# Kernel tuning notes

Measured on AMD Instinct MI355X. Metric: run time of the kernel, lower is better.

The kernel has to match this reference:

```python
import jax, jax.numpy as jnp
import numpy as np

N, E, U, L = 10000, 320000, 256, 3


def setup_inputs() -> dict:
    key = jax.random.key(0)
    ks = jax.random.split(key, 16)
    s = 0.05
    p = {}
    p["pos"] = jax.random.normal(ks[0], (N, 2), jnp.float32)
    p["edge_attr_in"] = jax.random.uniform(ks[1], (E, 1), jnp.float32)
    p["edge_index"] = jax.random.randint(ks[2], (2, E), 0, N)
    p["Wp"] = jax.random.normal(ks[3], (2, U), jnp.float32) * s
    p["bp"] = jnp.zeros((U,), jnp.float32)
    p["Wa"] = jax.random.normal(ks[4], (1, U), jnp.float32) * s
    p["ba"] = jnp.zeros((U,), jnp.float32)
    p["W1"] = jax.random.normal(ks[5], (L, U, U), jnp.float32) * s
    p["b1"] = jnp.zeros((L, U), jnp.float32)
    p["W2"] = jax.random.normal(ks[6], (L, U, U), jnp.float32) * s
    p["b2"] = jnp.zeros((L, U), jnp.float32)
    p["We"] = jax.random.normal(ks[7], (L + 1, U, U), jnp.float32) * s
    p["be"] = jnp.zeros((L + 1, U), jnp.float32)
    p["Ws"] = jax.random.normal(ks[8], (L + 1, U, U), jnp.float32) * s
    p["Wt"] = jax.random.normal(ks[9], (L + 1, U, U), jnp.float32) * s
    p["Wm1"] = jax.random.normal(ks[10], (U + 1, U // 2), jnp.float32) * s
    p["bm1"] = jnp.zeros((U // 2,), jnp.float32)
    p["alpha"] = 0.25 * jnp.ones((1,), jnp.float32)  # PReLU default slope
    p["Wm2"] = jax.random.normal(ks[11], (U // 2, 1), jnp.float32) * s
    p["bm2"] = jnp.zeros((1,), jnp.float32)
    return p


def _forward(pos, edge_attr_in, edge_index, Wp, bp, Wa, ba, W1, b1, W2, b2,
             We, be, Ws, Wt, Wm1, bm1, alpha, Wm2, bm2):
    src, dst = edge_index[0], edge_index[1]
    x = pos @ Wp + bp                      # [N, U]
    e = edge_attr_in @ Wa + ba             # [E, U]

    def edge_update(x, e, l):
        # ResEdgeLinear: residual edge update from endpoint nodes + edge feats
        return e + jax.nn.relu(e @ We[l] + x[src] @ Ws[l] + x[dst] @ Wt[l] + be[l])

    for l in range(L):
        # ResNodeConv: gated gather-linear-scatter with residual
        gate = jax.nn.sigmoid(e)                                   # [E, U]
        msg = gate * (x[src] @ W2[l] + b2[l])                      # [E, U]
        agg = jax.ops.segment_sum(msg, dst, num_segments=N)        # [N, U]
        x_new = x + jax.nn.relu(x @ W1[l] + b1[l] + agg)
        e_new = edge_update(x, e, l)  # simultaneous update: both use old (x, e)
        x, e = x_new, e_new
    e = edge_update(x, e, L)

    h = jnp.concatenate([e, edge_attr_in[:, :1]], axis=-1) @ Wm1 + bm1
    h = jnp.where(h > 0, h, alpha * h)  # PReLU
    return h @ Wm2 + bm2                # [E, 1] logits


def reference(pos, edge_attr_in, edge_index, Wp, bp, Wa, ba, W1, b1, W2, b2,
              We, be, Ws, Wt, Wm1, bm1, alpha, Wm2, bm2):
    return _forward(pos, edge_attr_in, edge_index, Wp, bp, Wa, ba, W1, b1,
                    W2, b2, We, be, Ws, Wt, Wm1, bm1, alpha, Wm2, bm2)
```

## Files before the change

kernel.cpp:

```cpp
#include <hip/hip_runtime.h>
#include <hip/hip_bf16.h>
#include <stdint.h>

#define N_NODES 10000
#define N_EDGES 320000

using bf16x8 = __attribute__((ext_vector_type(8))) short;
using fp32x4 = __attribute__((ext_vector_type(4))) float;
using u16x8 = __attribute__((ext_vector_type(8))) unsigned short;
using i32x4 = __attribute__((ext_vector_type(4))) int;

__device__ __forceinline__ float bf2f(unsigned short u) {
  union { unsigned int i; float f; } v; v.i = ((unsigned int)u) << 16; return v.f;
}
__device__ __forceinline__ unsigned short f2bf(float f) {
  union { float f; unsigned int i; } v; v.f = f;
  unsigned int x = v.i;
  x += 0x7fffu + ((x >> 16) & 1u);
  return (unsigned short)(x >> 16);
}
__device__ __forceinline__ unsigned int f2bf_pk(float lo, float hi) {
  __hip_bfloat162 h = __float22bfloat162_rn(float2{lo, hi});
  union { __hip_bfloat162 h; unsigned int u; } cv; cv.h = h; return cv.u;
}

#define A_POS 0
#define A_EA 20000
#define A_WP 340000
#define A_BP 340512
#define A_WA 340768
#define A_BA 341024
#define A_W1 341280
#define A_B1 537888
#define A_W2 538656
#define A_B2 735264
#define A_WE 736032
#define A_BE 998176
#define A_WS 999200
#define A_WT 1261344
#define A_WM1 1523488
#define A_BM1 1556384
#define A_AL 1556512
#define A_WM2 1556544
#define A_BM2 1556672
#define ARENA_USED 1556673
#define ARENA_TOT 1556736

__constant__ int g_off[19] = {A_POS, A_EA, A_WP, A_BP, A_WA, A_BA, A_W1, A_B1,
                              A_W2, A_B2, A_WE, A_BE, A_WS, A_WT, A_WM1,
                              A_BM1, A_AL, A_WM2, A_BM2};

struct Ptrs { const void* p[19]; };

__global__ void k_detect(const unsigned short* wpraw, int* flag, int* deg) {
  int i = blockIdx.x * 256 + threadIdx.x;
  if (i < N_NODES) deg[i] = 0;
  if (blockIdx.x == 0) {
    __shared__ int cnt;
    int tid = threadIdx.x;
    if (tid == 0) cnt = 0;
    __syncthreads();
    float v0 = bf2f(wpraw[tid]);
    float v1 = bf2f(wpraw[256 + tid]);
    int big = (fabsf(v0) > 100.f ? 1 : 0) + (fabsf(v1) > 100.f ? 1 : 0);
    atomicAdd(&cnt, big);
    __syncthreads();
    if (tid == 0) *flag = (cnt > 10) ? 1 : 0;
  }
}

__global__ void k_cast(Ptrs ptrs, const int* __restrict__ flag,
                       unsigned short* __restrict__ arena) {
  int a = blockIdx.x * 256 + threadIdx.x;
  if (a >= ARENA_USED) return;
  int z = 0;
#pragma unroll
  for (int j = 1; j < 19; ++j) if (a >= g_off[j]) z = j;
  int i = a - g_off[z];
  float v;
  if (*flag) v = ((const float*)ptrs.p[z])[i];
  else       v = bf2f(((const unsigned short*)ptrs.p[z])[i]);
  arena[a] = f2bf(v);
}

__global__ void k_prep(const unsigned short* __restrict__ arena,
                       unsigned short* nodeBT, unsigned short* WeT,
                       unsigned short* Wm1T, unsigned short* biascat) {
  int z = blockIdx.z;
  int i = blockIdx.x * 256 + threadIdx.x;
  if (z == 19) {
    if (i < 3072) {
      int l = i >> 10, j = i & 1023;
      unsigned short v = 0;
      if (j < 256) v = arena[A_B1 + l * 256 + j];
      else if (j < 512) v = arena[A_B2 + l * 256 + (j - 256)];
      biascat[i] = v;
    } else if (i < 3584) {
      biascat[i] = 0;
    }
    return;
  }
  const unsigned short* src; unsigned short* dst; int srcN = 256;
  if (z < 3)       {                 src = arena + A_W1 + z * 65536; dst = nodeBT + z * 262144; }
  else if (z < 6)  { int l = z - 3;  src = arena + A_W2 + l * 65536; dst = nodeBT + l * 262144 + 65536; }
  else if (z < 10) { int l = z - 6;  src = arena + A_WS + l * 65536;
                     dst = (l < 3) ? nodeBT + l * 262144 + 131072 : nodeBT + 786432; }
  else if (z < 14) { int l = z - 10; src = arena + A_WT + l * 65536;
                     dst = (l < 3) ? nodeBT + l * 262144 + 196608 : nodeBT + 786432 + 65536; }
  else if (z < 18) { int l = z - 14; src = arena + A_WE + l * 65536; dst = WeT + l * 65536; }
  else             { src = arena + A_WM1; dst = Wm1T; srcN = 128; }
  if (i < srcN * 256) {
    int k = i & 255, n = i >> 8;
    dst[i] = src[k * srcN + n];
  }
}

__global__ void k_pack(const unsigned short* __restrict__ src,
                       unsigned short* __restrict__ dst, int MT, int nchunks) {
  int c = blockIdx.x * 256 + threadIdx.x;
  if (c >= nchunks) return;
  int perg = MT * 512;
  int g = c / perg, r = c % perg;
  int ks = r / (64 * MT);
  int rem = r % (64 * MT);
  int mt = rem >> 6, lane = rem & 63;
  int q = lane >> 4, ll = lane & 15;
  int oc = g * (MT * 16) + (ll >> 2) * (MT * 4) + (ll & 3) + mt * 4;
  i32x4 v = *(const i32x4*)((const char*)src + ((long)oc << 9) + (ks << 6) + (q << 4));
  ((i32x4*)dst)[c] = v;
}

__global__ void k_init_x(const unsigned short* __restrict__ arena,
                         float* __restrict__ xf, unsigned short* __restrict__ xbf,
                         float* __restrict__ agg) {
  int n = blockIdx.x, c = threadIdx.x;
  float p0 = bf2f(arena[A_POS + 2 * n]), p1 = bf2f(arena[A_POS + 2 * n + 1]);
  float v = fmaf(p0, bf2f(arena[A_WP + c]),
                 fmaf(p1, bf2f(arena[A_WP + 256 + c]), bf2f(arena[A_BP + c])));
  long idx = ((long)n << 8) + c;
  xf[idx] = v;
  xbf[idx] = f2bf(v);
  agg[idx] = 0.f;
}

__global__ void k_hist(const int* __restrict__ dstA, int* __restrict__ deg) {
  int i = blockIdx.x * 256 + threadIdx.x;
  if (i < N_EDGES) {
    int d = dstA[i];
    if ((unsigned)d < N_NODES) atomicAdd(&deg[d], 1);
  }
}

__global__ void k_scan(const int* __restrict__ deg, int* __restrict__ rowptr,
                       int* __restrict__ cursor) {
  __shared__ int part[256];
  int tid = threadIdx.x;
  int base = tid * 40;
  int s = 0;
  for (int i = 0; i < 40; ++i) {
    int idx = base + i;
    if (idx < N_NODES) s += deg[idx];
  }
  part[tid] = s;
  __syncthreads();
  if (tid == 0) {
    int run = 0;
    for (int i = 0; i < 256; ++i) { int t = part[i]; part[i] = run; run += t; }
    rowptr[N_NODES] = run;
  }
  __syncthreads();
  int run = part[tid];
  for (int i = 0; i < 40; ++i) {
    int idx = base + i;
    if (idx < N_NODES) { rowptr[idx] = run; cursor[idx] = run; run += deg[idx]; }
  }
}

__global__ void k_fill(const int* __restrict__ dstA, const int* __restrict__ srcA,
                       const unsigned short* __restrict__ arena,
                       int* __restrict__ cursor, int* __restrict__ eid,
                       int* __restrict__ csrc, int* __restrict__ cdst,
                       unsigned short* __restrict__ eaC) {
  int i = blockIdx.x * 256 + threadIdx.x;
  if (i < N_EDGES) {
    int d = dstA[i]; if ((unsigned)d >= N_NODES) d = 0;
    int p = atomicAdd(&cursor[d], 1);
    if ((unsigned)p < N_EDGES) {
      eid[p] = i;
      int s = srcA[i]; if ((unsigned)s >= N_NODES) s = 0;
      csrc[p] = s;
      cdst[p] = d;
      eaC[p] = arena[A_EA + i];
    }
  }
}

#define SM_PITCH 528
#define XS_PITCH 144
#define EDGE_BLOCKS (N_EDGES / 128)

template <bool NT, int ROWS, int BLK>
__device__ __forceinline__ void stage_tile(char* smc, const unsigned short* src,
                                           long rowBase) {
  int tid = threadIdx.x;
#pragma unroll
  for (int it = 0; it < ROWS * 32 / BLK; ++it) {
    int lin = it * BLK + tid;
    int row = lin >> 5, g = lin & 31;
    const i32x4* p = (const i32x4*)((const char*)src + ((rowBase + row) << 9) + (g << 4));
    i32x4 v = NT ? __builtin_nontemporal_load(p) : *p;
    *(i32x4*)(smc + row * SM_PITCH + (g << 4)) = v;
  }
}

template <int MT, int NTT>
__device__ __forceinline__ void gemm_swap(const char* smc, const unsigned short* WTp,
                                          int colBase, fp32x4 (&acc)[MT][NTT]) {
  const int lane = threadIdx.x & 63;
  const int q = lane >> 4, ll = lane & 15;
  const char* wbase = (const char*)WTp + ((long)colBase << 9) + (lane << 4);
  __builtin_amdgcn_s_setprio(1);
#pragma unroll
  for (int ks = 0; ks < 8; ++ks) {
    bf16x8 a[MT];
#pragma unroll
    for (int mt = 0; mt < MT; ++mt)
      a[mt] = *(const bf16x8*)(wbase + ((long)(ks * MT + mt) << 10));
    bf16x8 b[NTT];
#pragma unroll
    for (int nt = 0; nt < NTT; ++nt)
      b[nt] = *(const bf16x8*)(smc + (nt * 16 + ll) * SM_PITCH + (ks << 6) + (q << 4));
#pragma unroll
    for (int mt = 0; mt < MT; ++mt)
#pragma unroll
      for (int nt = 0; nt < NTT; ++nt)
        acc[mt][nt] = __builtin_amdgcn_mfma_f32_16x16x32_bf16(a[mt], b[nt], acc[mt][nt], 0, 0, 0);
  }
  __builtin_amdgcn_s_setprio(0);
}

template <int NTT>
__device__ __forceinline__ void edge_epilogue_cx(
    char* smc, char* xsw, const fp32x4 (&acc)[4][NTT], const int* s_src,
    const int* s_dst, const unsigned short* XW, int xw_pitch, int xs_off,
    int xt_off, const unsigned short* bePtr, int colBase, int lane) {
  const int q = lane >> 4, ll = lane & 15;
  const int cb = colBase + q * 16;
  u16x8 be0 = *(const u16x8*)(bePtr + cb);
  u16x8 be1 = *(const u16x8*)(bePtr + cb + 8);
  const int prow = lane >> 3;
  const int ppc = lane & 7;
  const int pcol = xs_off + colBase + ppc * 8;
  u16x8 pfA = *(const u16x8*)(XW + (long)s_src[prow] * xw_pitch + pcol);
  u16x8 pfB = *(const u16x8*)(XW + (long)s_src[8 + prow] * xw_pitch + pcol);
#pragma unroll
  for (int nt = 0; nt < NTT; ++nt) {
    *(u16x8*)(xsw + prow * XS_PITCH + ppc * 16) = pfA;
    *(u16x8*)(xsw + (8 + prow) * XS_PITCH + ppc * 16) = pfB;
    if (nt + 1 < NTT) {
      int elA = (nt + 1) * 16 + prow;
      pfA = *(const u16x8*)(XW + (long)s_src[elA] * xw_pitch + pcol);
      pfB = *(const u16x8*)(XW + (long)s_src[elA + 8] * xw_pitch + pcol);
    }
    int el = nt * 16 + ll;
    int dn = s_dst[el];
    const unsigned short* xtrow = XW + (long)dn * xw_pitch + xt_off + cb;
    u16x8 xt0 = *(const u16x8*)(xtrow);
    u16x8 xt1 = *(const u16x8*)(xtrow + 8);
    u16x8 xs0 = *(const u16x8*)(xsw + ll * XS_PITCH + q * 32);
    u16x8 xs1 = *(const u16x8*)(xsw + ll * XS_PITCH + q * 32 + 16);
    u16x8* slot = (u16x8*)(smc + el * SM_PITCH + cb * 2);
    u16x8 er0 = slot[0], er1 = slot[1];
    float f[16];
#pragma unroll
    for (int mt = 0; mt < 4; ++mt)
#pragma unroll
      for (int r = 0; r < 4; ++r) {
        int i = mt * 4 + r;
        float xsv = bf2f(i < 8 ? xs0[i] : xs1[i - 8]);
        float xtv = bf2f(i < 8 ? xt0[i] : xt1[i - 8]);
        float erv = bf2f(i < 8 ? er0[i] : er1[i - 8]);
        float bev = bf2f(i < 8 ? be0[i] : be1[i - 8]);
        float v = acc[mt][nt][r] + xsv + xtv + bev;
        v = fmaxf(v, 0.f);
        f[i] = erv + v;
      }
    union { u16x8 v; unsigned int w[4]; } O0, O1;
#pragma unroll
    for (int p = 0; p < 4; ++p) {
      O0.w[p] = f2bf_pk(f[2 * p], f[2 * p + 1]);
      O1.w[p] = f2bf_pk(f[8 + 2 * p], f[9 + 2 * p]);
    }
    slot[0] = O0.v;
    slot[1] = O1.v;
  }
}

template <int MODE>
__global__ __launch_bounds__(256, 2) void k_fat(
    unsigned short* __restrict__ e, const unsigned short* __restrict__ WT_edge,
    const unsigned short* __restrict__ XW_edge,
    const unsigned short* __restrict__ bePtr, const unsigned short* __restrict__ arena,
    const unsigned short* __restrict__ eaC,
    const int* __restrict__ csrc, const int* __restrict__ cdst,
    const unsigned short* __restrict__ xbf, const unsigned short* __restrict__ WT_node,
    const unsigned short* __restrict__ bias, unsigned short* __restrict__ XW_out) {
  __shared__ int4 sm4[128 * 33];
  __shared__ int4 xsb4[4 * 2304 / 16];
  __shared__ int s_src[128];
  __shared__ int s_dst[128];
  char* smc = (char*)sm4;
  const int tid = threadIdx.x;
  const int wave = tid >> 6, lane = tid & 63;
  const int q = lane >> 4, ll = lane & 15;

  if (blockIdx.x < EDGE_BLOCKS) {
    const long tileBase = (long)blockIdx.x * 128;
    const int colBase = wave * 64;
    if (MODE == 0) {
#pragma unroll
      for (int it = 0; it < 16; ++it) {
        int lin = it * 256 + tid;
        int row = lin >> 5, g = lin & 31;
        float eav = bf2f(eaC[tileBase + row]);
        int c0 = g * 8;
        float f[8];
#pragma unroll
        for (int j = 0; j < 8; ++j)
          f[j] = fmaf(eav, bf2f(arena[A_WA + c0 + j]), bf2f(arena[A_BA + c0 + j]));
        union { bf16x8 v; unsigned int w[4]; } O;
#pragma unroll
        for (int p = 0; p < 4; ++p) O.w[p] = f2bf_pk(f[2 * p], f[2 * p + 1]);
        *(bf16x8*)(smc + row * SM_PITCH + (g << 4)) = O.v;
      }
    } else {
      stage_tile<true, 128, 256>(smc, e, tileBase);
    }
    if (tid < 128) {
      long edge = tileBase + tid;
      int s = csrc[edge]; if ((unsigned)s >= N_NODES) s = 0;
      int d = cdst[edge]; if ((unsigned)d >= N_NODES) d = 0;
      s_src[tid] = s;
      s_dst[tid] = d;
    }
    __syncthreads();

    fp32x4 acc[4][8];
#pragma unroll
    for (int mt = 0; mt < 4; ++mt)
#pragma unroll
      for (int nt = 0; nt < 8; ++nt) acc[mt][nt] = 0.f;
    gemm_swap<4, 8>(smc, WT_edge, colBase, acc);
    __syncthreads();

    edge_epilogue_cx<8>(smc, (char*)xsb4 + wave * 2304, acc, s_src, s_dst,
                        XW_edge, 1024, 512, 768, bePtr, colBase, lane);
    __syncthreads();

#pragma unroll
    for (int it = 0; it < 16; ++it) {
      int lin = it * 256 + tid;
      int row = lin >> 5, g = lin & 31;
      i32x4 v = *(const i32x4*)(smc + row * SM_PITCH + (g << 4));
      __builtin_nontemporal_store(v, (i32x4*)((char*)e + ((tileBase + row) << 9) + (g << 4)));
    }
  } else {
    int b = blockIdx.x - EDGE_BLOCKS;
    int bx = b % 79, by = b / 79;
    const long tileBase = (long)bx * 128;
#pragma unroll
    for (int it = 0; it < 16; ++it) {
      int lin = it * 256 + tid;
      int row = lin >> 5, g = lin & 31;
      long rg = tileBase + row;
      if (rg > N_NODES - 1) rg = N_NODES - 1;
      i32x4 v = *(const i32x4*)((const char*)xbf + (rg << 9) + (g << 4));
      *(i32x4*)(smc + row * SM_PITCH + (g << 4)) = v;
    }
    __syncthreads();
    fp32x4 acc[2][8];
#pragma unroll
    for (int mt = 0; mt < 2; ++mt)
#pragma unroll
      for (int nt = 0; nt < 8; ++nt) acc[mt][nt] = 0.f;
    const int colBase = by * 128 + wave * 32;
    gemm_swap<2, 8>(smc, WT_node, colBase, acc);

    const int cb = colBase + q * 8;
    u16x8 bs8 = *(const u16x8*)(bias + cb);
#pragma unroll
    for (int nt = 0; nt < 8; ++nt) {
      long nn = tileBase + nt * 16 + ll;
      if (nn >= N_NODES) continue;
      float f[8];
#pragma unroll
      for (int mt = 0; mt < 2; ++mt)
#pragma unroll
        for (int r = 0; r < 4; ++r) {
          int i = mt * 4 + r;
          f[i] = acc[mt][nt][r] + bf2f(bs8[i]);
        }
      union { u16x8 v; unsigned int w[4]; } O;
#pragma unroll
      for (int p = 0; p < 4; ++p) O.w[p] = f2bf_pk(f[2 * p], f[2 * p + 1]);
      *(u16x8*)(XW_out + nn * 1024 + cb) = O.v;
    }
  }
}

__global__ __launch_bounds__(256, 2) void k_edge_last2(
    const unsigned short* __restrict__ e, const unsigned short* __restrict__ WeT2,
    const unsigned short* __restrict__ WeT3,
    const unsigned short* __restrict__ XW2, const unsigned short* __restrict__ XW3,
    const unsigned short* __restrict__ arena, const unsigned short* __restrict__ eaC,
    const int* __restrict__ csrc, const int* __restrict__ cdst,
    const unsigned short* __restrict__ Wm1T, const int* __restrict__ eid,
    const int* __restrict__ flag, void* __restrict__ out) {
  __shared__ int4 sm4[128 * 33];
  __shared__ int4 xsb4[4 * 2304 / 16];
  __shared__ int s_src[128];
  __shared__ int s_dst[128];
  char* smc = (char*)sm4;
  const long tileBase = (long)blockIdx.x * 128;
  const int tid = threadIdx.x;
  const int wave = tid >> 6, lane = tid & 63;
  const int q = lane >> 4, ll = lane & 15;
  const int colBase = wave * 64;
  char* xsw = (char*)xsb4 + wave * 2304;

  stage_tile<true, 128, 256>(smc, e, tileBase);
  if (tid < 128) {
    long edge = tileBase + tid;
    int s = csrc[edge]; if ((unsigned)s >= N_NODES) s = 0;
    int d = cdst[edge]; if ((unsigned)d >= N_NODES) d = 0;
    s_src[tid] = s;
    s_dst[tid] = d;
  }
  __syncthreads();

  fp32x4 acc[4][8];
#pragma unroll
  for (int mt = 0; mt < 4; ++mt)
#pragma unroll
    for (int nt = 0; nt < 8; ++nt) acc[mt][nt] = 0.f;
  gemm_swap<4, 8>(smc, WeT2, colBase, acc);
  __syncthreads();
  edge_epilogue_cx<8>(smc, xsw, acc, s_src, s_dst, XW2, 1024, 512, 768,
                      arena + A_BE + 2 * 256, colBase, lane);
  __syncthreads();

#pragma unroll
  for (int mt = 0; mt < 4; ++mt)
#pragma unroll
    for (int nt = 0; nt < 8; ++nt) acc[mt][nt] = 0.f;
  gemm_swap<4, 8>(smc, WeT3, colBase, acc);
  __syncthreads();
  edge_epilogue_cx<8>(smc, xsw, acc, s_src, s_dst, XW3, 512, 0, 256,
                      arena + A_BE + 3 * 256, colBase, lane);
  __syncthreads();

  fp32x4 acc2[2][8];
#pragma unroll
  for (int mt = 0; mt < 2; ++mt)
#pragma unroll
    for (int nt = 0; nt < 8; ++nt) acc2[mt][nt] = 0.f;
  const int colBase2 = wave * 32;
  gemm_swap<2, 8>(smc, Wm1T, colBase2, acc2);

  const int cb2 = colBase2 + q * 8;
  float alphaf = bf2f(arena[A_AL]);
  float bmc[8], wl[8], w2c[8];
#pragma unroll
  for (int i = 0; i < 8; ++i) {
    bmc[i] = bf2f(arena[A_BM1 + cb2 + i]);
    wl[i] = bf2f(arena[A_WM1 + 32768 + cb2 + i]);
    w2c[i] = bf2f(arena[A_WM2 + cb2 + i]);
  }
  __syncthreads();
  float* part = (float*)smc;
#pragma unroll
  for (int nt = 0; nt < 8; ++nt) {
    int el = nt * 16 + ll;
    float eav = bf2f(eaC[tileBase + el]);
    float ps = 0.f;
#pragma unroll
    for (int mt = 0; mt < 2; ++mt)
#pragma unroll
      for (int r = 0; r < 4; ++r) {
        int i = mt * 4 + r;
        float h = acc2[mt][nt][r] + bmc[i] + eav * wl[i];
        h = (h > 0.f) ? h : alphaf * h;
        ps += h * w2c[i];
      }
    ps += __shfl_xor(ps, 16, 64);
    ps += __shfl_xor(ps, 32, 64);
    if (q == 0) part[el * 4 + wave] = ps;
  }
  __syncthreads();
  if (tid < 128) {
    float t = part[tid * 4] + part[tid * 4 + 1] + part[tid * 4 + 2] + part[tid * 4 + 3]
            + bf2f(arena[A_BM2]);
    long row = tileBase + tid;
    int oe = eid[row]; if ((unsigned)oe >= N_EDGES) oe = 0;
    if (*flag) ((float*)out)[oe] = t;
    else       ((unsigned short*)out)[oe] = f2bf(t);
  }
}

__global__ __launch_bounds__(256, 2) void k_node_gemm(
    const unsigned short* __restrict__ xbf, const unsigned short* __restrict__ WT,
    const unsigned short* __restrict__ bias, unsigned short* __restrict__ out,
    int out_pitch) {
  __shared__ int4 sm4[128 * 33];
  char* smc = (char*)sm4;
  const long tileBase = (long)blockIdx.x * 128;
  {
    int tid = threadIdx.x;
#pragma unroll
    for (int it = 0; it < 16; ++it) {
      int lin = it * 256 + tid;
      int row = lin >> 5, g = lin & 31;
      long rg = tileBase + row;
      if (rg > N_NODES - 1) rg = N_NODES - 1;
      i32x4 v = *(const i32x4*)((const char*)xbf + (rg << 9) + (g << 4));
      *(i32x4*)(smc + row * SM_PITCH + (g << 4)) = v;
    }
  }
  __syncthreads();
  fp32x4 acc[2][8];
#pragma unroll
  for (int mt = 0; mt < 2; ++mt)
#pragma unroll
    for (int nt = 0; nt < 8; ++nt) acc[mt][nt] = 0.f;
  const int tid = threadIdx.x, wave = tid >> 6, lane = tid & 63;
  const int q = lane >> 4, ll = lane & 15;
  const int colBase = blockIdx.y * 128 + wave * 32;
  gemm_swap<2, 8>(smc, WT, colBase, acc);

  const int cb = colBase + q * 8;
  u16x8 bs8 = *(const u16x8*)(bias + cb);
#pragma unroll
  for (int nt = 0; nt < 8; ++nt) {
    long nn = tileBase + nt * 16 + ll;
    if (nn >= N_NODES) continue;
    float f[8];
#pragma unroll
    for (int mt = 0; mt < 2; ++mt)
#pragma unroll
      for (int r = 0; r < 4; ++r) {
        int i = mt * 4 + r;
        f[i] = acc[mt][nt][r] + bf2f(bs8[i]);
      }
    union { u16x8 v; unsigned int w[4]; } O;
#pragma unroll
    for (int p = 0; p < 4; ++p) O.w[p] = f2bf_pk(f[2 * p], f[2 * p + 1]);
    *(u16x8*)(out + nn * out_pitch + cb) = O.v;
  }
}

template <bool FIRST>
__global__ void k_agg(const int* __restrict__ csrc, const int* __restrict__ cdst,
                      const unsigned short* __restrict__ e,
                      const unsigned short* __restrict__ eaC,
                      const unsigned short* __restrict__ arena,
                      const unsigned short* __restrict__ XW, int xw_pitch, int x2_off,
                      float* __restrict__ agg) {
  __shared__ int s_src[64];
  __shared__ int s_dst[64];
  const long base = (long)blockIdx.x * 64;
  const int c = threadIdx.x;
  if (c < 64) {
    long r = base + c;
    int s = csrc[r]; if ((unsigned)s >= N_NODES) s = 0;
    int d = cdst[r]; if ((unsigned)d >= N_NODES) d = 0;
    s_src[c] = s;
    s_dst[c] = d;
  }
  __syncthreads();
  float wac = 0.f, bac = 0.f;
  if (FIRST) { wac = bf2f(arena[A_WA + c]); bac = bf2f(arena[A_BA + c]); }
  float a = 0.f;
  int run = s_dst[0];
  for (int b8 = 0; b8 < 64; b8 += 8) {
    float evv[8], x2v[8];
#pragma unroll
    for (int j = 0; j < 8; ++j) {
      int row = b8 + j;
      if (FIRST) evv[j] = fmaf(bf2f(eaC[base + row]), wac, bac);
      else evv[j] = bf2f(__builtin_nontemporal_load(e + ((base + row) << 8) + c));
      x2v[j] = bf2f(XW[(long)s_src[row] * xw_pitch + x2_off + c]);
    }
#pragma unroll
    for (int j = 0; j < 8; ++j) {
      int d = s_dst[b8 + j];
      if (d != run) {
        atomicAdd(&agg[((long)run << 8) + c], a);
        a = 0.f;
        run = d;
      }
      float gate = 1.f / (1.f + __expf(-evv[j]));
      a = fmaf(gate, x2v[j], a);
    }
  }
  atomicAdd(&agg[((long)run << 8) + c], a);
}

__global__ void k_node_update(float* __restrict__ xf, unsigned short* __restrict__ xbf,
                              const unsigned short* __restrict__ XW,
                              float* __restrict__ agg) {
  int n = blockIdx.x, c = threadIdx.x;
  long idx = ((long)n << 8) + c;
  float av = agg[idx];
  agg[idx] = 0.f;
  float t = bf2f(XW[((long)n << 10) + c]) + av;
  float nx = xf[idx] + fmaxf(t, 0.f);
  xf[idx] = nx;
  xbf[idx] = f2bf(nx);
}

extern "C" void kernel_launch(void* const* d_in, const int* in_sizes, int n_in,
                              void* d_out, int out_size, void* d_ws, size_t ws_size,
                              hipStream_t stream) {
  const int* eidx = (const int*)d_in[2];
  const int* srcA = eidx;
  const int* dstA = eidx + N_EDGES;
  (void)in_sizes; (void)n_in; (void)out_size;

  char* ws = (char*)d_ws;
  size_t off = 0;
  auto alloc = [&](size_t bytes) -> char* {
    char* p = ws + off;
    off = (off + bytes + 255) & ~(size_t)255;
    return p;
  };
  unsigned short* e_buf   = (unsigned short*)alloc((size_t)N_EDGES * 256 * 2);
  float*          xf      = (float*)alloc((size_t)N_NODES * 256 * 4);
  unsigned short* xbf     = (unsigned short*)alloc((size_t)N_NODES * 256 * 2);
  unsigned short* XWa     = (unsigned short*)alloc((size_t)N_NODES * 1024 * 2);
  unsigned short* XWb     = (unsigned short*)alloc((size_t)N_NODES * 1024 * 2);
  unsigned short* XW3     = (unsigned short*)alloc((size_t)N_NODES * 512 * 2);
  float*          agg     = (float*)alloc((size_t)N_NODES * 256 * 4);
  unsigned short* nodeBT  = (unsigned short*)alloc((size_t)917504 * 2);
  unsigned short* WeT     = (unsigned short*)alloc((size_t)4 * 65536 * 2);
  unsigned short* Wm1T    = (unsigned short*)alloc((size_t)32768 * 2);
  unsigned short* nodeBTp = (unsigned short*)alloc((size_t)917504 * 2);
  unsigned short* WeTp    = (unsigned short*)alloc((size_t)4 * 65536 * 2);
  unsigned short* Wm1Tp   = (unsigned short*)alloc((size_t)32768 * 2);
  unsigned short* biascat = (unsigned short*)alloc((size_t)3584 * 2);
  unsigned short* arena   = (unsigned short*)alloc((size_t)ARENA_TOT * 2);
  int* deg    = (int*)alloc((size_t)N_NODES * 4);
  int* rowptr = (int*)alloc((size_t)(N_NODES + 1) * 4);
  int* cursor = (int*)alloc((size_t)N_NODES * 4);
  int* eid    = (int*)alloc((size_t)N_EDGES * 4);
  int* csrc   = (int*)alloc((size_t)N_EDGES * 4);
  int* cdst   = (int*)alloc((size_t)N_EDGES * 4);
  unsigned short* eaC = (unsigned short*)alloc((size_t)N_EDGES * 2);
  int* flag   = (int*)alloc(4);
  if (ws_size < off) return;

  Ptrs ptrs;
  {
    int map[19] = {0, 1, 3, 4, 5, 6, 7, 8, 9, 10, 11, 12, 13, 14, 15, 16, 17, 18, 19};
    for (int j = 0; j < 19; ++j) ptrs.p[j] = d_in[map[j]];
  }

  dim3 blk(256);
  k_detect<<<dim3(40), blk, 0, stream>>>((const unsigned short*)d_in[3], flag, deg);
  k_cast<<<dim3((ARENA_USED + 255) / 256), blk, 0, stream>>>(ptrs, flag, arena);
  k_prep<<<dim3(256, 1, 20), blk, 0, stream>>>(arena, nodeBT, WeT, Wm1T, biascat);
  k_pack<<<dim3(448), blk, 0, stream>>>(nodeBT, nodeBTp, 2, 114688);
  k_pack<<<dim3(128), blk, 0, stream>>>(WeT, WeTp, 4, 32768);
  k_pack<<<dim3(16),  blk, 0, stream>>>(Wm1T, Wm1Tp, 2, 4096);
  k_init_x<<<dim3(N_NODES), blk, 0, stream>>>(arena, xf, xbf, agg);
  k_hist<<<dim3(N_EDGES / 256), blk, 0, stream>>>(dstA, deg);
  k_scan<<<dim3(1), blk, 0, stream>>>(deg, rowptr, cursor);
  k_fill<<<dim3(N_EDGES / 256), blk, 0, stream>>>(dstA, srcA, arena, cursor, eid, csrc,
                                                  cdst, eaC);

  k_node_gemm<<<dim3(79, 8), blk, 0, stream>>>(xbf, nodeBTp, biascat, XWa, 1024);
  k_agg<true><<<dim3(N_EDGES / 64), blk, 0, stream>>>(csrc, cdst, e_buf, eaC, arena,
                                                      XWa, 1024, 256, agg);
  k_node_update<<<dim3(N_NODES), blk, 0, stream>>>(xf, xbf, XWa, agg);
  k_fat<0><<<dim3(EDGE_BLOCKS + 632), blk, 0, stream>>>(
      e_buf, WeTp, XWa, arena + A_BE, arena, eaC, csrc, cdst,
      xbf, nodeBTp + 262144, biascat + 1024, XWb);
  k_agg<false><<<dim3(N_EDGES / 64), blk, 0, stream>>>(csrc, cdst, e_buf, eaC, arena,
                                                       XWb, 1024, 256, agg);
  k_node_update<<<dim3(N_NODES), blk, 0, stream>>>(xf, xbf, XWb, agg);
  k_fat<1><<<dim3(EDGE_BLOCKS + 632), blk, 0, stream>>>(
      e_buf, WeTp + 65536, XWb, arena + A_BE + 256, arena, eaC, csrc, cdst,
      xbf, nodeBTp + 2 * 262144, biascat + 2048, XWa);
  k_agg<false><<<dim3(N_EDGES / 64), blk, 0, stream>>>(csrc, cdst, e_buf, eaC, arena,
                                                       XWa, 1024, 256, agg);
  k_node_update<<<dim3(N_NODES), blk, 0, stream>>>(xf, xbf, XWa, agg);
  k_node_gemm<<<dim3(79, 4), blk, 0, stream>>>(xbf, nodeBTp + 786432, biascat + 3072, XW3, 512);
  k_edge_last2<<<dim3(EDGE_BLOCKS), blk, 0, stream>>>(
      e_buf, WeTp + 2 * 65536, WeTp + 3 * 65536, XWa, XW3, arena, eaC,
      csrc, cdst, Wm1Tp, eid, flag, d_out);
}
```

Baseline: 789.1 us.

## Fuse edge layers 0 and 1 with in-tile gated aggregation, splitting node GEMMs out

Layer-0 and layer-1 edge updates now run in one kernel, with the edge tile kept in shared memory between the two edge GEMMs instead of being written to and re-read from global memory. The layer-1 gated message aggregation is done in the same kernel, using the freshly computed layer-1 edge features and run-length merged atomicAdds over the dst-sorted edges, which removes one k_agg launch and its reread of e. The node GEMMs that used to share the fat kernels now run as separate k_node_gemm launches. The cost is more atomics and gathers inside the fused kernel, and the loss of overlap between node and edge GEMMs.

New measurement: 777.1 us. Within noise of the previous version (-1.5%).

```diff
diff --git a/kernel.cpp b/kernel.cpp
--- a/kernel.cpp
+++ b/kernel.cpp
@@ -296,115 +296,102 @@
   }
 }
 
-template <int MODE>
-__global__ __launch_bounds__(256, 2) void k_fat(
-    unsigned short* __restrict__ e, const unsigned short* __restrict__ WT_edge,
-    const unsigned short* __restrict__ XW_edge,
-    const unsigned short* __restrict__ bePtr, const unsigned short* __restrict__ arena,
-    const unsigned short* __restrict__ eaC,
+__global__ __launch_bounds__(256, 2) void k_edge01(
+    unsigned short* __restrict__ e, const unsigned short* __restrict__ WeT0,
+    const unsigned short* __restrict__ WeT1,
+    const unsigned short* __restrict__ XWa, const unsigned short* __restrict__ XWb,
+    const unsigned short* __restrict__ arena, const unsigned short* __restrict__ eaC,
     const int* __restrict__ csrc, const int* __restrict__ cdst,
-    const unsigned short* __restrict__ xbf, const unsigned short* __restrict__ WT_node,
-    const unsigned short* __restrict__ bias, unsigned short* __restrict__ XW_out) {
+    float* __restrict__ agg) {
   __shared__ int4 sm4[128 * 33];
   __shared__ int4 xsb4[4 * 2304 / 16];
   __shared__ int s_src[128];
   __shared__ int s_dst[128];
   char* smc = (char*)sm4;
+  const long tileBase = (long)blockIdx.x * 128;
   const int tid = threadIdx.x;
   const int wave = tid >> 6, lane = tid & 63;
-  const int q = lane >> 4, ll = lane & 15;
-
-  if (blockIdx.x < EDGE_BLOCKS) {
-    const long tileBase = (long)blockIdx.x * 128;
-    const int colBase = wave * 64;
-    if (MODE == 0) {
-#pragma unroll
-      for (int it = 0; it < 16; ++it) {
-        int lin = it * 256 + tid;
-        int row = lin >> 5, g = lin & 31;
-        float eav = bf2f(eaC[tileBase + row]);
-        int c0 = g * 8;
-        float f[8];
-#pragma unroll
-        for (int j = 0; j < 8; ++j)
-          f[j] = fmaf(eav, bf2f(arena[A_WA + c0 + j]), bf2f(arena[A_BA + c0 + j]));
-        union { bf16x8 v; unsigned int w[4]; } O;
-#pragma unroll
-        for (int p = 0; p < 4; ++p) O.w[p] = f2bf_pk(f[2 * p], f[2 * p + 1]);
-        *(bf16x8*)(smc + row * SM_PITCH + (g << 4)) = O.v;
+  const int colBase = wave * 64;
+  char* xsw = (char*)xsb4 + wave * 2304;
+
+#pragma unroll
+  for (int it = 0; it < 16; ++it) {
+    int lin = it * 256 + tid;
+    int row = lin >> 5, g = lin & 31;
+    float eav = bf2f(eaC[tileBase + row]);
+    int c0 = g * 8;
+    float f[8];
+#pragma unroll
+    for (int j = 0; j < 8; ++j)
+      f[j] = fmaf(eav, bf2f(arena[A_WA + c0 + j]), bf2f(arena[A_BA + c0 + j]));
+    union { bf16x8 v; unsigned int w[4]; } O;
+#pragma unroll
+    for (int p = 0; p < 4; ++p) O.w[p] = f2bf_pk(f[2 * p], f[2 * p + 1]);
+    *(bf16x8*)(smc + row * SM_PITCH + (g << 4)) = O.v;
+  }
+  if (tid < 128) {
+    long edge = tileBase + tid;
+    int s = csrc[edge]; if ((unsigned)s >= N_NODES) s = 0;
+    int d = cdst[edge]; if ((unsigned)d >= N_NODES) d = 0;
+    s_src[tid] = s;
+    s_dst[tid] = d;
+  }
+  __syncthreads();
+
+  fp32x4 acc[4][8];
+#pragma unroll
+  for (int mt = 0; mt < 4; ++mt)
+#pragma unroll
+    for (int nt = 0; nt < 8; ++nt) acc[mt][nt] = 0.f;
+  gemm_swap<4, 8>(smc, WeT0, colBase, acc);
+  __syncthreads();
+  edge_epilogue_cx<8>(smc, xsw, acc, s_src, s_dst, XWa, 1024, 512, 768,
+                      arena + A_BE, colBase, lane);
+  __syncthreads();
+
+  {
+    const int c = tid;
+    float a = 0.f;
+    int run = s_dst[0];
+    for (int b8 = 0; b8 < 128; b8 += 8) {
+      float evv[8], x2v[8];
+#pragma unroll
+      for (int j = 0; j < 8; ++j) {
+        int row = b8 + j;
+        evv[j] = bf2f(*(const unsigned short*)(smc + row * SM_PITCH + c * 2));
+        x2v[j] = bf2f(XWb[(long)s_src[row] * 1024 + 256 + c]);
       }
-    } else {
-      stage_tile<true, 128, 256>(smc, e, tileBase);
-    }
-    if (tid < 128) {
-      long edge = tileBase + tid;
-      int s = csrc[edge]; if ((unsigned)s >= N_NODES) s = 0;
-      int d = cdst[edge]; if ((unsigned)d >= N_NODES) d = 0;
-      s_src[tid] = s;
-      s_dst[tid] = d;
-    }
-    __syncthreads();
-
-    fp32x4 acc[4][8];
-#pragma unroll
-    for (int mt = 0; mt < 4; ++mt)
-#pragma unroll
-      for (int nt = 0; nt < 8; ++nt) acc[mt][nt] = 0.f;
-    gemm_swap<4, 8>(smc, WT_edge, colBase, acc);
-    __syncthreads();
-
-    edge_epilogue_cx<8>(smc, (char*)xsb4 + wave * 2304, acc, s_src, s_dst,
-                        XW_edge, 1024, 512, 768, bePtr, colBase, lane);
-    __syncthreads();
-
-#pragma unroll
-    for (int it = 0; it < 16; ++it) {
-      int lin = it * 256 + tid;
-      int row = lin >> 5, g = lin & 31;
-      i32x4 v = *(const i32x4*)(smc + row * SM_PITCH + (g << 4));
-      __builtin_nontemporal_store(v, (i32x4*)((char*)e + ((tileBase + row) << 9) + (g << 4)));
-    }
-  } else {
-    int b = blockIdx.x - EDGE_BLOCKS;
-    int bx = b % 79, by = b / 79;
-    const long tileBase = (long)bx * 128;
-#pragma unroll
-    for (int it = 0; it < 16; ++it) {
-      int lin = it * 256 + tid;
-      int row = lin >> 5, g = lin & 31;
-      long rg = tileBase + row;
-      if (rg > N_NODES - 1) rg = N_NODES - 1;
-      i32x4 v = *(const i32x4*)((const char*)xbf + (rg << 9) + (g << 4));
-      *(i32x4*)(smc + row * SM_PITCH + (g << 4)) = v;
-    }
-    __syncthreads();
-    fp32x4 acc[2][8];
-#pragma unroll
-    for (int mt = 0; mt < 2; ++mt)
-#pragma unroll
-      for (int nt = 0; nt < 8; ++nt) acc[mt][nt] = 0.f;
-    const int colBase = by * 128 + wave * 32;
-    gemm_swap<2, 8>(smc, WT_node, colBase, acc);
-
-    const int cb = colBase + q * 8;
-    u16x8 bs8 = *(const u16x8*)(bias + cb);
-#pragma unroll
-    for (int nt = 0; nt < 8; ++nt) {
-      long nn = tileBase + nt * 16 + ll;
-      if (nn >= N_NODES) continue;
-      float f[8];
-#pragma unroll
-      for (int mt = 0; mt < 2; ++mt)
-#pragma unroll
-        for (int r = 0; r < 4; ++r) {
-          int i = mt * 4 + r;
-          f[i] = acc[mt][nt][r] + bf2f(bs8[i]);
+#pragma unroll
+      for (int j = 0; j < 8; ++j) {
+        int d = s_dst[b8 + j];
+        if (d != run) {
+          atomicAdd(&agg[((long)run << 8) + c], a);
+          a = 0.f;
+          run = d;
         }
-      union { u16x8 v; unsigned int w[4]; } O;
-#pragma unroll
-      for (int p = 0; p < 4; ++p) O.w[p] = f2bf_pk(f[2 * p], f[2 * p + 1]);
-      *(u16x8*)(XW_out + nn * 1024 + cb) = O.v;
-    }
+        float gate = 1.f / (1.f + __expf(-evv[j]));
+        a = fmaf(gate, x2v[j], a);
+      }
+    }
+    atomicAdd(&agg[((long)run << 8) + c], a);
+  }
+
+#pragma unroll
+  for (int mt = 0; mt < 4; ++mt)
+#pragma unroll
+    for (int nt = 0; nt < 8; ++nt) acc[mt][nt] = 0.f;
+  gemm_swap<4, 8>(smc, WeT1, colBase, acc);
+  __syncthreads();
+  edge_epilogue_cx<8>(smc, xsw, acc, s_src, s_dst, XWb, 1024, 512, 768,
+                      arena + A_BE + 256, colBase, lane);
+  __syncthreads();
+
+#pragma unroll
+  for (int it = 0; it < 16; ++it) {
+    int lin = it * 256 + tid;
+    int row = lin >> 5, g = lin & 31;
+    i32x4 v = *(const i32x4*)(smc + row * SM_PITCH + (g << 4));
+    __builtin_nontemporal_store(v, (i32x4*)((char*)e + ((tileBase + row) << 9) + (g << 4)));
   }
 }
 
@@ -681,15 +668,13 @@
   k_agg<true><<<dim3(N_EDGES / 64), blk, 0, stream>>>(csrc, cdst, e_buf, eaC, arena,
                                                       XWa, 1024, 256, agg);
   k_node_update<<<dim3(N_NODES), blk, 0, stream>>>(xf, xbf, XWa, agg);
-  k_fat<0><<<dim3(EDGE_BLOCKS + 632), blk, 0, stream>>>(
-      e_buf, WeTp, XWa, arena + A_BE, arena, eaC, csrc, cdst,
-      xbf, nodeBTp + 262144, biascat + 1024, XWb);
-  k_agg<false><<<dim3(N_EDGES / 64), blk, 0, stream>>>(csrc, cdst, e_buf, eaC, arena,
-                                                       XWb, 1024, 256, agg);
+  k_node_gemm<<<dim3(79, 8), blk, 0, stream>>>(xbf, nodeBTp + 262144, biascat + 1024,
+                                               XWb, 1024);
+  k_edge01<<<dim3(EDGE_BLOCKS), blk, 0, stream>>>(
+      e_buf, WeTp, WeTp + 65536, XWa, XWb, arena, eaC, csrc, cdst, agg);
   k_node_update<<<dim3(N_NODES), blk, 0, stream>>>(xf, xbf, XWb, agg);
-  k_fat<1><<<dim3(EDGE_BLOCKS + 632), blk, 0, stream>>>(
-      e_buf, WeTp + 65536, XWb, arena + A_BE + 256, arena, eaC, csrc, cdst,
-      xbf, nodeBTp + 2 * 262144, biascat + 2048, XWa);
+  k_node_gemm<<<dim3(79, 8), blk, 0, stream>>>(xbf, nodeBTp + 2 * 262144, biascat + 2048,
+                                               XWa, 1024);
   k_agg<false><<<dim3(N_EDGES / 64), blk, 0, stream>>>(csrc, cdst, e_buf, eaC, arena,
                                                        XWa, 1024, 256, agg);
   k_node_update<<<dim3(N_NODES), blk, 0, stream>>>(xf, xbf, XWa, agg);
```
